# Performance work log

Measured on AMD Instinct MI355X. Metric: run time of the kernel, lower is better.

Reference implementation:

```python
import jax, jax.numpy as jnp
import numpy as np

N = 100000
E = 1600000
D_IN = 128
D_HID = 128
D_OUT = 64


def setup_inputs() -> dict:
    key = jax.random.key(0)
    ks = jax.random.split(key, 9)
    x = jax.random.normal(ks[0], (N, D_IN), dtype=jnp.float32)
    edge_index = jax.random.randint(ks[1], (2, E), 0, N, dtype=jnp.int64)
    edge_weight = jax.random.uniform(ks[2], (E,), dtype=jnp.float32)
    s1 = 1.0 / np.sqrt(D_IN)
    s2 = 1.0 / np.sqrt(D_HID)
    W1 = jax.random.uniform(ks[3], (D_IN, D_HID), jnp.float32, -s1, s1)
    b1 = jnp.zeros((D_HID,), jnp.float32)
    W2 = jax.random.uniform(ks[4], (D_HID, D_HID), jnp.float32, -s2, s2)
    b2 = jnp.zeros((D_HID,), jnp.float32)
    Wfc = jax.random.uniform(ks[5], (D_HID, D_OUT), jnp.float32, -s2, s2)
    bfc = jax.random.uniform(ks[6], (D_OUT,), jnp.float32, -s2, s2)
    return {"x": x, "edge_index": edge_index, "edge_weight": edge_weight,
            "W1": W1, "b1": b1, "W2": W2, "b2": b2, "Wfc": Wfc, "bfc": bfc}


def _gcn_layer(h, row, col, w, n, W, b):
    # h' = D^{-1/2} (A + I) D^{-1/2} h W + b  (PyG GCNConv with edge weights)
    h = h @ W  # [n, d_out]
    deg = jax.ops.segment_sum(w, col, num_segments=n)  # weighted in-degree incl. self loops
    dinv = jnp.where(deg > 0, jax.lax.rsqrt(deg), 0.0)
    norm = dinv[row] * w * dinv[col]  # [E+n]
    out = jax.ops.segment_sum(norm[:, None] * h[row], col, num_segments=n)
    return out + b


def reference(x, edge_index, edge_weight, W1, b1, W2, b2, Wfc, bfc):
    n = x.shape[0]
    loop = jnp.arange(n, dtype=edge_index.dtype)
    row = jnp.concatenate([edge_index[0], loop])  # sources (+ self loops)
    col = jnp.concatenate([edge_index[1], loop])  # destinations
    w = jnp.concatenate([edge_weight, jnp.ones((n,), edge_weight.dtype)])
    h = jax.nn.relu(_gcn_layer(x, row, col, w, n, W1, b1))
    h = jax.nn.relu(_gcn_layer(h, row, col, w, n, W2, b2))
    return jax.nn.sigmoid(h @ Wfc + bfc)
```

## Files before the change

### kernel.cpp

```cpp
#include <hip/hip_runtime.h>
#include <math.h>

#define N_NODES 100000
#define N_EDGES 1600000
#define SCAN_CHUNK 1024
#define NSCAN ((N_NODES + SCAN_CHUNK - 1) / SCAN_CHUNK)
#define WMASK ((1ull << 40) - 1)

__device__ __forceinline__ float2 bf2f(unsigned int u) {
    float2 r;
    r.x = __uint_as_float(u << 16);
    r.y = __uint_as_float(u & 0xffff0000u);
    return r;
}
__device__ __forceinline__ unsigned int f2bf2(float a, float b) {
    unsigned int ua = __float_as_uint(a), ub = __float_as_uint(b);
    ua += 0x7fffu + ((ua >> 16) & 1u);
    ub += 0x7fffu + ((ub >> 16) & 1u);
    return (ua >> 16) | (ub & 0xffff0000u);
}

__global__ void k_detect(const int* __restrict__ ei, int* __restrict__ flag, int host_hint) {
    __shared__ int s_cnt;
    if (threadIdx.x == 0) s_cnt = 0;
    __syncthreads();
    int local = 0;
    for (int e = threadIdx.x; e < 4096; e += blockDim.x)
        if (ei[2 * e + 1] != 0) local++;
    atomicAdd(&s_cnt, local);
    __syncthreads();
    if (threadIdx.x == 0) flag[0] = (host_hint || s_cnt < 100) ? 1 : 0;
}

__global__ void k_init(unsigned long long* __restrict__ packed) {
    int i = blockIdx.x * blockDim.x + threadIdx.x;
    if (i < N_NODES) packed[i] = 0ull;
}

__global__ void k_hist(const int* __restrict__ ei32, const int* __restrict__ flag,
                       const float* __restrict__ w,
                       unsigned long long* __restrict__ packed) {
    int e = blockIdx.x * blockDim.x + threadIdx.x;
    if (e >= N_EDGES) return;
    int c;
    if (flag[0]) {
        const long long* ei64 = (const long long*)ei32;
        c = (int)ei64[N_EDGES + e];
    } else {
        c = ei32[N_EDGES + e];
    }
    unsigned long long wfix = (unsigned long long)(w[e] * 4294967296.0f);
    atomicAdd(&packed[c], (1ull << 40) | wfix);
}

__global__ __launch_bounds__(256) void k_scan_a(const unsigned long long* __restrict__ packed,
                                                int* __restrict__ cnt,
                                                float* __restrict__ dinv,
                                                int* __restrict__ bsum) {
    __shared__ int sred[4];
    const int b = blockIdx.x, tid = threadIdx.x;
    const int base = b * SCAN_CHUNK;
    int s = 0;
    #pragma unroll
    for (int i = 0; i < 4; i++) {
        int idx = base + tid + i * 256;
        if (idx < N_NODES) {
            unsigned long long p = packed[idx];
            int c = (int)(p >> 40);
            float deg = 1.0f + (float)(p & WMASK) * 2.3283064365386963e-10f;
            cnt[idx] = c;
            dinv[idx] = rsqrtf(deg);
            s += c;
        }
    }
    #pragma unroll
    for (int sh = 1; sh < 64; sh <<= 1) s += __shfl_xor(s, sh);
    if ((tid & 63) == 0) sred[tid >> 6] = s;
    __syncthreads();
    if (tid == 0) bsum[b] = sred[0] + sred[1] + sred[2] + sred[3];
}

__global__ __launch_bounds__(128) void k_scan_b(const int* __restrict__ bsum,
                                                int* __restrict__ bex) {
    __shared__ int wsum[2];
    const int tid = threadIdx.x, lane = tid & 63, w = tid >> 6;
    int v = (tid < NSCAN) ? bsum[tid] : 0;
    int x = v;
    #pragma unroll
    for (int sh = 1; sh < 64; sh <<= 1) {
        int t = __shfl_up(x, sh);
        if (lane >= sh) x += t;
    }
    if (lane == 63) wsum[w] = x;
    __syncthreads();
    int add = (w == 1) ? wsum[0] : 0;
    if (tid < NSCAN) bex[tid] = x - v + add;
}

__global__ __launch_bounds__(256) void k_scan_c(const int* __restrict__ cnt,
                                                const int* __restrict__ bex,
                                                int* __restrict__ off,
                                                int* __restrict__ cur) {
    __shared__ int swave[4];
    const int b = blockIdx.x, tid = threadIdx.x;
    const int base = b * SCAN_CHUNK + tid * 4;
    int4 v = make_int4(0, 0, 0, 0);
    if (base + 3 < N_NODES) v = *(const int4*)&cnt[base];
    else {
        if (base + 0 < N_NODES) v.x = cnt[base + 0];
        if (base + 1 < N_NODES) v.y = cnt[base + 1];
        if (base + 2 < N_NODES) v.z = cnt[base + 2];
    }
    const int tsum = v.x + v.y + v.z + v.w;
    const int lane = tid & 63, w = tid >> 6;
    int x = tsum;
    #pragma unroll
    for (int sh = 1; sh < 64; sh <<= 1) {
        int t = __shfl_up(x, sh);
        if (lane >= sh) x += t;
    }
    if (lane == 63) swave[w] = x;
    __syncthreads();
    int wadd = 0;
    for (int i = 0; i < w; i++) wadd += swave[i];
    const int ex = bex[b] + wadd + (x - tsum);
    const int p0 = ex, p1 = p0 + v.x, p2 = p1 + v.y, p3 = p2 + v.z;
    if (base + 3 < N_NODES) {
        *(int4*)&off[base] = make_int4(p0, p1, p2, p3);
        *(int4*)&cur[base] = make_int4(p0, p1, p2, p3);
    } else {
        if (base + 0 < N_NODES) { off[base + 0] = p0; cur[base + 0] = p0; }
        if (base + 1 < N_NODES) { off[base + 1] = p1; cur[base + 1] = p1; }
        if (base + 2 < N_NODES) { off[base + 2] = p2; cur[base + 2] = p2; }
    }
}

__global__ void k_scatter(const int* __restrict__ ei32, const int* __restrict__ flag,
                          const float* __restrict__ w, const float* __restrict__ dinv,
                          int* __restrict__ cursor, unsigned int* __restrict__ sedge) {
    int e = blockIdx.x * blockDim.x + threadIdx.x;
    if (e >= N_EDGES) return;
    int r, c;
    if (flag[0]) {
        const long long* ei64 = (const long long*)ei32;
        r = (int)ei64[e];
        c = (int)ei64[N_EDGES + e];
    } else {
        r = ei32[e];
        c = ei32[N_EDGES + e];
    }
    float coef = dinv[r] * w[e] * dinv[c];
    unsigned int q = (unsigned int)(coef * 32767.0f + 0.5f);
    int p = atomicAdd(&cursor[c], 1);
    sedge[p] = ((unsigned int)r << 15) | q;
}

template <int DOUT, bool SIG, bool OBF16>
__global__ __launch_bounds__(256) void k_gemm(const float* __restrict__ A,
                                              const float* __restrict__ W,
                                              const float* __restrict__ bias,
                                              void* __restrict__ Cv) {
    constexpr int CPT = DOUT / 16;
    __shared__ float Ws[128 * DOUT];
    __shared__ float As[8][128];
    const int tid = threadIdx.x;
    const int tx = tid & 15, ty = tid >> 4;

    for (int i = tid * 4; i < 128 * DOUT; i += 256 * 4)
        *(float4*)&Ws[i] = *(const float4*)&W[i];

    const int r0 = blockIdx.x * 128;
    const int arow = tid >> 1;
    const int ak = (tid & 1) * 4;
    const bool rowok = (r0 + arow) < N_NODES;

    float acc[8][CPT];
    #pragma unroll
    for (int i = 0; i < 8; i++)
        #pragma unroll
        for (int j = 0; j < CPT; j++) acc[i][j] = 0.f;

    for (int k0 = 0; k0 < 128; k0 += 8) {
        float4 av = make_float4(0.f, 0.f, 0.f, 0.f);
        if (rowok) av = *(const float4*)&A[(size_t)(r0 + arow) * 128 + k0 + ak];
        __syncthreads();
        As[ak + 0][arow] = av.x;
        As[ak + 1][arow] = av.y;
        As[ak + 2][arow] = av.z;
        As[ak + 3][arow] = av.w;
        __syncthreads();
        #pragma unroll
        for (int kk = 0; kk < 8; kk++) {
            float4 a0 = *(const float4*)&As[kk][ty * 8];
            float4 a1 = *(const float4*)&As[kk][ty * 8 + 4];
            float av8[8] = {a0.x, a0.y, a0.z, a0.w, a1.x, a1.y, a1.z, a1.w};
            float wv[CPT];
            float4 w0 = *(const float4*)&Ws[(k0 + kk) * DOUT + tx * CPT];
            wv[0] = w0.x; wv[1] = w0.y; wv[2] = w0.z; wv[3] = w0.w;
            if constexpr (CPT == 8) {
                float4 w1 = *(const float4*)&Ws[(k0 + kk) * DOUT + tx * CPT + 4];
                wv[4] = w1.x; wv[5] = w1.y; wv[6] = w1.z; wv[7] = w1.w;
            }
            #pragma unroll
            for (int i = 0; i < 8; i++)
                #pragma unroll
                for (int j = 0; j < CPT; j++)
                    acc[i][j] = fmaf(av8[i], wv[j], acc[i][j]);
        }
    }

    #pragma unroll
    for (int i = 0; i < 8; i++) {
        int r = r0 + ty * 8 + i;
        if (r < N_NODES) {
            if constexpr (OBF16) {
                unsigned int* Cb = (unsigned int*)Cv;
                uint4 pk;
                pk.x = f2bf2(acc[i][0], acc[i][1]);
                pk.y = f2bf2(acc[i][2], acc[i][3]);
                pk.z = f2bf2(acc[i][4], acc[i][5]);
                pk.w = f2bf2(acc[i][6], acc[i][7]);
                *(uint4*)&Cb[(size_t)r * 64 + tx * 4] = pk;
            } else {
                float* C = (float*)Cv;
                float vout[CPT];
                #pragma unroll
                for (int j = 0; j < CPT; j++) {
                    float v = acc[i][j];
                    if constexpr (SIG) {
                        v += bias[tx * CPT + j];
                        v = 1.0f / (1.0f + expf(-v));
                    }
                    vout[j] = v;
                }
                #pragma unroll
                for (int j = 0; j < CPT; j += 4)
                    *(float4*)&C[(size_t)r * DOUT + tx * CPT + j] =
                        make_float4(vout[j], vout[j + 1], vout[j + 2], vout[j + 3]);
            }
        }
    }
}

__global__ __launch_bounds__(256) void k_aggregate(const unsigned int* __restrict__ lin,
                                                   const unsigned int* __restrict__ sedge,
                                                   const int* __restrict__ off,
                                                   const int* __restrict__ cnt,
                                                   const float* __restrict__ dinv,
                                                   const float* __restrict__ bias,
                                                   float* __restrict__ out) {
    const int node = (blockIdx.x * 256 + threadIdx.x) >> 6;
    const int lane = threadIdx.x & 63;
    if (node >= N_NODES) return;
    const float di = dinv[node];
    float2 sv = bf2f(lin[(size_t)node * 64 + lane]);
    float ax = di * di * sv.x;
    float ay = di * di * sv.y;
    const int start = __builtin_amdgcn_readfirstlane(off[node]);
    const int end = start + __builtin_amdgcn_readfirstlane(cnt[node]);
    for (int e0 = start; e0 < end; e0 += 8) {
        unsigned int en[8];
        #pragma unroll
        for (int i = 0; i < 8; i++) {
            int idx = e0 + i;
            en[i] = sedge[idx < end ? idx : end - 1];
        }
        float2 v[8];
        #pragma unroll
        for (int i = 0; i < 8; i++)
            v[i] = bf2f(lin[(size_t)(en[i] >> 15) * 64 + lane]);
        #pragma unroll
        for (int i = 0; i < 8; i++) {
            float cf = (e0 + i < end) ? (float)(en[i] & 0x7fffu) * 3.051850947599719e-05f : 0.0f;
            ax = fmaf(cf, v[i].x, ax);
            ay = fmaf(cf, v[i].y, ay);
        }
    }
    const int lane2 = lane * 2;
    float2 bv = *(const float2*)&bias[lane2];
    ax = fmaxf(ax + bv.x, 0.f);
    ay = fmaxf(ay + bv.y, 0.f);
    *(float2*)&out[(size_t)node * 128 + lane2] = make_float2(ax, ay);
}

extern "C" void kernel_launch(void* const* d_in, const int* in_sizes, int n_in,
                              void* d_out, int out_size, void* d_ws, size_t ws_size,
                              hipStream_t stream) {
    const float* x   = (const float*)d_in[0];
    const int*   ei  = (const int*)d_in[1];
    const float* ew  = (const float*)d_in[2];
    const float* W1  = (const float*)d_in[3];
    const float* b1  = (const float*)d_in[4];
    const float* W2  = (const float*)d_in[5];
    const float* b2  = (const float*)d_in[6];
    const float* Wfc = (const float*)d_in[7];
    const float* bfc = (const float*)d_in[8];
    float* out = (float*)d_out;

    char* ws = (char*)d_ws;
    size_t o = 0;
    auto alloc = [&](size_t bytes) { char* p = ws + o; o += (bytes + 255) & ~255ull; return p; };
    unsigned long long* packed = (unsigned long long*)alloc((size_t)N_NODES * 8);
    float* dinv  = (float*)alloc((size_t)N_NODES * 4);
    int*   cnt   = (int*)  alloc((size_t)N_NODES * 4);
    int*   off   = (int*)  alloc((size_t)N_NODES * 4);
    int*   cur   = (int*)  alloc((size_t)N_NODES * 4);
    int*   flag  = (int*)  alloc(256);
    int*   bsum  = (int*)  alloc((size_t)NSCAN * 4);
    int*   bex   = (int*)  alloc((size_t)NSCAN * 4);
    unsigned int* sedge = (unsigned int*)alloc((size_t)N_EDGES * 4);
    unsigned int* hbf   = (unsigned int*)alloc((size_t)N_NODES * 64 * 4);
    float*        aggf  = (float*)alloc((size_t)N_NODES * 128 * 4);

    const int EB = (N_EDGES + 255) / 256;
    const int NB = (N_NODES + 255) / 256;

    int hint64 = (in_sizes[1] == 4 * N_EDGES) ? 1 : 0;
    k_detect<<<1, 256, 0, stream>>>(ei, flag, hint64);
    k_init<<<NB, 256, 0, stream>>>(packed);
    k_hist<<<EB, 256, 0, stream>>>(ei, flag, ew, packed);
    k_scan_a<<<NSCAN, 256, 0, stream>>>(packed, cnt, dinv, bsum);
    k_scan_b<<<1, 128, 0, stream>>>(bsum, bex);
    k_scan_c<<<NSCAN, 256, 0, stream>>>(cnt, bex, off, cur);
    k_scatter<<<EB, 256, 0, stream>>>(ei, flag, ew, dinv, cur, sedge);

    const int GB = (N_NODES + 127) / 128;
    const int AB = (N_NODES * 64 + 255) / 256;

    k_gemm<128, false, true><<<GB, 256, 0, stream>>>(x, W1, nullptr, hbf);
    k_aggregate<<<AB, 256, 0, stream>>>(hbf, sedge, off, cnt, dinv, b1, aggf);
    k_gemm<128, false, true><<<GB, 256, 0, stream>>>(aggf, W2, nullptr, hbf);
    k_aggregate<<<AB, 256, 0, stream>>>(hbf, sedge, off, cnt, dinv, b2, aggf);
    k_gemm<64, true, false><<<GB, 256, 0, stream>>>(aggf, Wfc, bfc, out);
}
```

Before: 563.4 us.

## Use bf16 MFMA GEMMs for the 128-wide layers and store layer-1 output in bf16

Replaces the two 128x128 FP32 SIMT GEMMs with an MFMA kernel (16x16x32 bf16). Weights are pre-transposed and cast to bf16, and the A tiles are staged in padded LDS. The first aggregation now writes bf16 so the second GEMM reads half the bytes, and the bias-free SIMT paths are removed. This is meant to cut GEMM compute and memory traffic, at the cost of extra bf16 rounding of activations and weights. The MFMA kernel also writes its output with scalar 2-byte stores.

After: 480.7 us. 14.7% less time.

```diff
diff --git a/kernel.cpp b/kernel.cpp
--- a/kernel.cpp
+++ b/kernel.cpp
@@ -6,6 +6,10 @@
 #define SCAN_CHUNK 1024
 #define NSCAN ((N_NODES + SCAN_CHUNK - 1) / SCAN_CHUNK)
 #define WMASK ((1ull << 40) - 1)
+#define LDSW 136
+
+typedef short bf16x8 __attribute__((ext_vector_type(8)));
+typedef float f32x4 __attribute__((ext_vector_type(4)));
 
 __device__ __forceinline__ float2 bf2f(unsigned int u) {
     float2 r;
@@ -18,6 +22,11 @@
     ua += 0x7fffu + ((ua >> 16) & 1u);
     ub += 0x7fffu + ((ub >> 16) & 1u);
     return (ua >> 16) | (ub & 0xffff0000u);
+}
+__device__ __forceinline__ unsigned short f2bf(float a) {
+    unsigned int u = __float_as_uint(a);
+    u += 0x7fffu + ((u >> 16) & 1u);
+    return (unsigned short)(u >> 16);
 }
 
 __global__ void k_detect(const int* __restrict__ ei, int* __restrict__ flag, int host_hint) {
@@ -155,11 +164,91 @@
     sedge[p] = ((unsigned int)r << 15) | q;
 }
 
-template <int DOUT, bool SIG, bool OBF16>
+__global__ void k_castw(const float* __restrict__ W, unsigned short* __restrict__ Wt) {
+    int i = blockIdx.x * blockDim.x + threadIdx.x;
+    int k = i >> 7, n = i & 127;
+    Wt[n * 128 + k] = f2bf(W[k * 128 + n]);
+}
+
+template <bool ABF16>
+__global__ __launch_bounds__(256) void k_gemm_mfma(const void* __restrict__ Av,
+                                                   const unsigned short* __restrict__ Wt,
+                                                   unsigned short* __restrict__ Cb) {
+    __shared__ unsigned short Al[128 * LDSW];
+    __shared__ unsigned short Wl[128 * LDSW];
+    const int tid = threadIdx.x;
+    const int srow = tid >> 1, h = tid & 1;
+    const int r0 = blockIdx.x * 128;
+
+    {
+        const uint4* src = (const uint4*)&Wt[srow * 128 + h * 64];
+        uint4* dst = (uint4*)&Wl[srow * LDSW + h * 64];
+        #pragma unroll
+        for (int c = 0; c < 8; c++) dst[c] = src[c];
+    }
+    {
+        const bool ok = (r0 + srow) < N_NODES;
+        uint4* dst = (uint4*)&Al[srow * LDSW + h * 64];
+        if constexpr (ABF16) {
+            const uint4* src = (const uint4*)((const unsigned short*)Av +
+                                              (size_t)(r0 + srow) * 128 + h * 64);
+            uint4 z = make_uint4(0, 0, 0, 0);
+            #pragma unroll
+            for (int c = 0; c < 8; c++) dst[c] = ok ? src[c] : z;
+        } else {
+            const float* src = (const float*)Av + (size_t)(r0 + srow) * 128 + h * 64;
+            #pragma unroll
+            for (int c = 0; c < 8; c++) {
+                float4 f0 = ok ? *(const float4*)&src[c * 8]     : make_float4(0, 0, 0, 0);
+                float4 f1 = ok ? *(const float4*)&src[c * 8 + 4] : make_float4(0, 0, 0, 0);
+                uint4 pk;
+                pk.x = f2bf2(f0.x, f0.y);
+                pk.y = f2bf2(f0.z, f0.w);
+                pk.z = f2bf2(f1.x, f1.y);
+                pk.w = f2bf2(f1.z, f1.w);
+                dst[c] = pk;
+            }
+        }
+    }
+    __syncthreads();
+
+    const int lane = tid & 63;
+    const int w = tid >> 6;
+    const int lr = lane & 15;
+    const int kg = lane >> 4;
+    f32x4 acc[2][8] = {};
+
+    #pragma unroll
+    for (int k0 = 0; k0 < 128; k0 += 32) {
+        const int kb = k0 + kg * 8;
+        bf16x8 a0 = *(const bf16x8*)&Al[(w * 32 + lr) * LDSW + kb];
+        bf16x8 a1 = *(const bf16x8*)&Al[(w * 32 + 16 + lr) * LDSW + kb];
+        #pragma unroll
+        for (int ct = 0; ct < 8; ct++) {
+            bf16x8 b = *(const bf16x8*)&Wl[(ct * 16 + lr) * LDSW + kb];
+            acc[0][ct] = __builtin_amdgcn_mfma_f32_16x16x32_bf16(a0, b, acc[0][ct], 0, 0, 0);
+            acc[1][ct] = __builtin_amdgcn_mfma_f32_16x16x32_bf16(a1, b, acc[1][ct], 0, 0, 0);
+        }
+    }
+
+    #pragma unroll
+    for (int rt = 0; rt < 2; rt++)
+        #pragma unroll
+        for (int r = 0; r < 4; r++) {
+            int row = r0 + w * 32 + rt * 16 + kg * 4 + r;
+            if (row < N_NODES) {
+                #pragma unroll
+                for (int ct = 0; ct < 8; ct++)
+                    Cb[(size_t)row * 128 + ct * 16 + lr] = f2bf(acc[rt][ct][r]);
+            }
+        }
+}
+
+template <int DOUT>
 __global__ __launch_bounds__(256) void k_gemm(const float* __restrict__ A,
                                               const float* __restrict__ W,
                                               const float* __restrict__ bias,
-                                              void* __restrict__ Cv) {
+                                              float* __restrict__ C) {
     constexpr int CPT = DOUT / 16;
     __shared__ float Ws[128 * DOUT];
     __shared__ float As[8][128];
@@ -197,10 +286,6 @@
             float wv[CPT];
             float4 w0 = *(const float4*)&Ws[(k0 + kk) * DOUT + tx * CPT];
             wv[0] = w0.x; wv[1] = w0.y; wv[2] = w0.z; wv[3] = w0.w;
-            if constexpr (CPT == 8) {
-                float4 w1 = *(const float4*)&Ws[(k0 + kk) * DOUT + tx * CPT + 4];
-                wv[4] = w1.x; wv[5] = w1.y; wv[6] = w1.z; wv[7] = w1.w;
-            }
             #pragma unroll
             for (int i = 0; i < 8; i++)
                 #pragma unroll
@@ -213,42 +298,28 @@
     for (int i = 0; i < 8; i++) {
         int r = r0 + ty * 8 + i;
         if (r < N_NODES) {
-            if constexpr (OBF16) {
-                unsigned int* Cb = (unsigned int*)Cv;
-                uint4 pk;
-                pk.x = f2bf2(acc[i][0], acc[i][1]);
-                pk.y = f2bf2(acc[i][2], acc[i][3]);
-                pk.z = f2bf2(acc[i][4], acc[i][5]);
-                pk.w = f2bf2(acc[i][6], acc[i][7]);
-                *(uint4*)&Cb[(size_t)r * 64 + tx * 4] = pk;
-            } else {
-                float* C = (float*)Cv;
-                float vout[CPT];
-                #pragma unroll
-                for (int j = 0; j < CPT; j++) {
-                    float v = acc[i][j];
-                    if constexpr (SIG) {
-                        v += bias[tx * CPT + j];
-                        v = 1.0f / (1.0f + expf(-v));
-                    }
-                    vout[j] = v;
-                }
-                #pragma unroll
-                for (int j = 0; j < CPT; j += 4)
-                    *(float4*)&C[(size_t)r * DOUT + tx * CPT + j] =
-                        make_float4(vout[j], vout[j + 1], vout[j + 2], vout[j + 3]);
+            float vout[CPT];
+            #pragma unroll
+            for (int j = 0; j < CPT; j++) {
+                float v = acc[i][j] + bias[tx * CPT + j];
+                vout[j] = 1.0f / (1.0f + expf(-v));
             }
-        }
-    }
-}
-
+            #pragma unroll
+            for (int j = 0; j < CPT; j += 4)
+                *(float4*)&C[(size_t)r * DOUT + tx * CPT + j] =
+                    make_float4(vout[j], vout[j + 1], vout[j + 2], vout[j + 3]);
+        }
+    }
+}
+
+template <bool OBF16>
 __global__ __launch_bounds__(256) void k_aggregate(const unsigned int* __restrict__ lin,
                                                    const unsigned int* __restrict__ sedge,
                                                    const int* __restrict__ off,
                                                    const int* __restrict__ cnt,
                                                    const float* __restrict__ dinv,
                                                    const float* __restrict__ bias,
-                                                   float* __restrict__ out) {
+                                                   void* __restrict__ outv) {
     const int node = (blockIdx.x * 256 + threadIdx.x) >> 6;
     const int lane = threadIdx.x & 63;
     if (node >= N_NODES) return;
@@ -280,7 +351,11 @@
     float2 bv = *(const float2*)&bias[lane2];
     ax = fmaxf(ax + bv.x, 0.f);
     ay = fmaxf(ay + bv.y, 0.f);
-    *(float2*)&out[(size_t)node * 128 + lane2] = make_float2(ax, ay);
+    if constexpr (OBF16) {
+        ((unsigned int*)outv)[(size_t)node * 64 + lane] = f2bf2(ax, ay);
+    } else {
+        *(float2*)&((float*)outv)[(size_t)node * 128 + lane2] = make_float2(ax, ay);
+    }
 }
 
 extern "C" void kernel_launch(void* const* d_in, const int* in_sizes, int n_in,
@@ -308,9 +383,12 @@
     int*   flag  = (int*)  alloc(256);
     int*   bsum  = (int*)  alloc((size_t)NSCAN * 4);
     int*   bex   = (int*)  alloc((size_t)NSCAN * 4);
-    unsigned int* sedge = (unsigned int*)alloc((size_t)N_EDGES * 4);
-    unsigned int* hbf   = (unsigned int*)alloc((size_t)N_NODES * 64 * 4);
-    float*        aggf  = (float*)alloc((size_t)N_NODES * 128 * 4);
+    unsigned int*   sedge = (unsigned int*)alloc((size_t)N_EDGES * 4);
+    unsigned short* W1t   = (unsigned short*)alloc(128 * 128 * 2);
+    unsigned short* W2t   = (unsigned short*)alloc(128 * 128 * 2);
+    unsigned short* hbf   = (unsigned short*)alloc((size_t)N_NODES * 128 * 2);
+    unsigned short* aggb  = (unsigned short*)alloc((size_t)N_NODES * 128 * 2);
+    float*          aggf  = (float*)alloc((size_t)N_NODES * 128 * 4);
 
     const int EB = (N_EDGES + 255) / 256;
     const int NB = (N_NODES + 255) / 256;
@@ -318,6 +396,8 @@
     int hint64 = (in_sizes[1] == 4 * N_EDGES) ? 1 : 0;
     k_detect<<<1, 256, 0, stream>>>(ei, flag, hint64);
     k_init<<<NB, 256, 0, stream>>>(packed);
+    k_castw<<<64, 256, 0, stream>>>(W1, W1t);
+    k_castw<<<64, 256, 0, stream>>>(W2, W2t);
     k_hist<<<EB, 256, 0, stream>>>(ei, flag, ew, packed);
     k_scan_a<<<NSCAN, 256, 0, stream>>>(packed, cnt, dinv, bsum);
     k_scan_b<<<1, 128, 0, stream>>>(bsum, bex);
@@ -327,9 +407,9 @@
     const int GB = (N_NODES + 127) / 128;
     const int AB = (N_NODES * 64 + 255) / 256;
 
-    k_gemm<128, false, true><<<GB, 256, 0, stream>>>(x, W1, nullptr, hbf);
-    k_aggregate<<<AB, 256, 0, stream>>>(hbf, sedge, off, cnt, dinv, b1, aggf);
-    k_gemm<128, false, true><<<GB, 256, 0, stream>>>(aggf, W2, nullptr, hbf);
-    k_aggregate<<<AB, 256, 0, stream>>>(hbf, sedge, off, cnt, dinv, b2, aggf);
-    k_gemm<64, true, false><<<GB, 256, 0, stream>>>(aggf, Wfc, bfc, out);
-}
+    k_gemm_mfma<false><<<GB, 256, 0, stream>>>(x, W1t, hbf);
+    k_aggregate<true><<<AB, 256, 0, stream>>>((const unsigned int*)hbf, sedge, off, cnt, dinv, b1, aggb);
+    k_gemm_mfma<true><<<GB, 256, 0, stream>>>(aggb, W2t, hbf);
+    k_aggregate<false><<<AB, 256, 0, stream>>>((const unsigned int*)hbf, sedge, off, cnt, dinv, b2, aggf);
+    k_gemm<64><<<GB, 256, 0, stream>>>(aggf, Wfc, bfc, out);
+}
```
